# Kernel tuning notes

Measured on AMD Instinct MI355X. Metric: run time of the kernel, lower is better.

The kernel has to match this reference:

```python
import jax, jax.numpy as jnp
import numpy as np

EP = 1e-4
MAX_ITER = 100
L = [512, 512]          # context lengths
C = 256                 # padded feature dim == total_dim
HEADS = 2


def nonsat_activation(x, ep=EP, max_iter=MAX_ITER):
    # Fixed-point iteration y <- (2y^3/3 + x)/(y^2+1), y0 = x.
    # Matches torch version: iterate on detached values, final update uses live x.
    xd = jax.lax.stop_gradient(x)
    f = lambda y: (2.0 * y ** 3 / 3.0 + xd) / (y ** 2 + 1.0)

    def cond(s):
        y, y_new, i = s
        return jnp.logical_and(jnp.mean(jnp.abs(y_new - y)) > ep, i <= max_iter)

    def body(s):
        y, y_new, i = s
        return (y_new, f(y_new), i + 1)

    y_prev, _, _ = jax.lax.while_loop(cond, body, (xd, f(xd), 0))
    y_prev = jax.lax.stop_gradient(y_prev)
    # final (returned) update, differentiable w.r.t. x only
    return (2.0 * y_prev ** 3 / 3.0 + x) / (y_prev ** 2 + 1.0)


def setup_inputs() -> dict:
    key = jax.random.key(0)
    k1, k2, k3 = jax.random.split(key, 3)
    x1 = jax.random.normal(k1, (32, 512, 256), dtype=jnp.float32)
    x2 = jax.random.normal(k2, (32, 512, 192), dtype=jnp.float32)
    # xavier_normal_ for U: std = sqrt(2/(fan_in+fan_out)) = sqrt(2/512) = 1/16
    U = jax.random.normal(k3, (HEADS, C, C), dtype=jnp.float32) * (1.0 / 16.0)
    return {"x1": x1, "x2": x2, "U": U}


def reference(x1, x2, U):
    # pad contexts to common feature dim C (zeros on the right)
    contexts = [x1, jnp.pad(x2, ((0, 0), (0, 0), (0, C - x2.shape[-1])))]
    q = sum(L)
    scaling = C ** (-0.5)
    M = jnp.concatenate(contexts, axis=1)  # (B, q, C)

    # mask uses sizes = L[1:] with blocks starting at offset 0 (faithful quirk)
    mask_mul = jnp.ones((q, q), dtype=jnp.float32).at[:L[1], :L[1]].set(0.0)

    h_reps = []
    mask_add = None
    for h in range(HEADS):
        # K[b,i,j] = sum_{c,d} M[b,i,c] U[h,c,d] M[b,j,d]
        K = jnp.einsum('bic,cd,bjd->bij', M, U[h], M) * scaling
        K = nonsat_activation(K)
        if mask_add is None:  # cached after head 0, reused for later heads
            mask_add = jnp.zeros((q, q), dtype=jnp.float32).at[:L[1], :L[1]].set(jnp.min(K))
        K_hat = K * mask_mul + mask_add
        cols = jnp.max(K_hat, axis=1)   # (B, q) max over rows per column
        rows = jnp.max(K_hat, axis=2)   # (B, q) max over cols per row
        alpha = rows + cols             # (B, q)
        reps = []
        offset = 0
        for i, Ci in enumerate(contexts):
            a = alpha[:, offset:offset + L[i]]          # (B, l_i)
            offset += L[i]
            wt = jax.nn.softmax(a, axis=1)              # (B, l_i)
            r = jnp.einsum('bl,blc->bc', wt, Ci)        # (B, C)
            reps.append(r)
        h_reps.append(jnp.stack(reps, axis=1))          # (B, N, C)
    return jnp.stack(h_reps, axis=0)                    # (heads, B, N, C)
```

## Files before the change

### kernel.cpp

```cpp
#include <hip/hip_runtime.h>
#include <math.h>

typedef _Float16 h16;
typedef h16  h16x8 __attribute__((ext_vector_type(8)));
typedef h16  h16x4 __attribute__((ext_vector_type(4)));
typedef float f32x4 __attribute__((ext_vector_type(4)));

#define MH_OFF   ((size_t)0)
#define ML_OFF   (MH_OFF + 16777216)
#define UHT_OFF  (ML_OFF + 16777216)
#define ULT_OFF  (UHT_OFF + 262144)
#define RMA_OFF  (ULT_OFF + 262144)
#define RMH_OFF  (RMA_OFF + 262144)
#define PCM_OFF  (RMH_OFF + 262144)
#define M0_OFF   (PCM_OFF + 4194304)

__device__ __forceinline__ float nonsat(float x) {
    float y = x;
#pragma unroll
    for (int i = 0; i < 24; ++i) {
        float y2 = y * y;
        y = fmaf(0.66666667f * y, y2, x) / (y2 + 1.0f);
    }
    return y;
}

__device__ __forceinline__ int fkey(float f) {
    const int i = __float_as_int(f);
    return (i >= 0) ? i : (i ^ 0x7fffffff);
}
__device__ __forceinline__ float funkey(int k) {
    return __int_as_float((k >= 0) ? k : (k ^ 0x7fffffff));
}

__global__ void k_prep(const float* __restrict__ x1, const float* __restrict__ x2,
                       const float* __restrict__ U, h16* __restrict__ MH,
                       h16* __restrict__ ML, h16* __restrict__ UHt,
                       h16* __restrict__ ULt, int* __restrict__ m0key,
                       float* __restrict__ out) {
    const int gid = blockIdx.x * 256 + threadIdx.x;
    if (blockIdx.x < 8192) {
        const int g  = gid;
        const int d4 = (g & 63) * 4;
        const int j  = (g >> 6) & 1023;
        const int b  = g >> 16;
        float v[4];
        if (j < 512) {
            const float4 p = *(const float4*)(x1 + ((size_t)(b * 512 + j) * 256 + d4));
            v[0] = p.x; v[1] = p.y; v[2] = p.z; v[3] = p.w;
        } else if (d4 < 192) {
            const float4 p = *(const float4*)(x2 +
                (size_t)(b * 512 + (j - 512)) * 192 + d4);
            v[0] = p.x; v[1] = p.y; v[2] = p.z; v[3] = p.w;
        } else {
            v[0] = v[1] = v[2] = v[3] = 0.0f;
        }
        h16x4 hh, ll;
#pragma unroll
        for (int k = 0; k < 4; ++k) {
            const h16 hi = (h16)v[k];
            hh[k] = hi;
            ll[k] = (h16)(v[k] - (float)hi);
        }
        const size_t o = (size_t)g * 4;
        *(h16x4*)&MH[o] = hh;
        *(h16x4*)&ML[o] = ll;
    } else if (blockIdx.x < 8320) {
        const int g  = gid - 8192 * 256;
        const int c4 = (g & 63) * 4;
        const int d  = (g >> 6) & 255;
        const int h  = g >> 14;
        h16x4 hh, ll;
#pragma unroll
        for (int k = 0; k < 4; ++k) {
            const float v = U[((size_t)h * 256 + c4 + k) * 256 + d] * 4.0f;
            const h16 hi = (h16)v;
            hh[k] = hi;
            ll[k] = (h16)(v - (float)hi);
        }
        const size_t o = ((size_t)h * 256 + d) * 256 + c4;
        *(h16x4*)&UHt[o] = hh;
        *(h16x4*)&ULt[o] = ll;
    } else {
        const int z = gid - 8320 * 256;
        out[z] = 0.0f;
        if (z == 0) *m0key = 0x7fffffff;
    }
}

__global__ __launch_bounds__(256, 2)
void k_main(const h16* __restrict__ MH, const h16* __restrict__ ML,
            const h16* __restrict__ UHt, const h16* __restrict__ ULt,
            float* __restrict__ rmax_all, float* __restrict__ rmax_hi,
            float* __restrict__ pcm, int* __restrict__ m0key) {
    __shared__ __align__(16) h16 sP[2][64 * 256];
    __shared__ float red[512 + 4];

    const int n    = blockIdx.x;
    const int x    = n & 7;
    const int s    = n >> 3;
    const int b    = x + 8 * (s >> 5);
    const int h    = (s >> 4) & 1;
    const int rblk = s & 15;
    const int hb   = h * 32 + b;
    const int r0   = rblk * 64;
    const int t    = threadIdx.x;
    const int w    = t >> 6;
    const int l    = t & 63;
    const int q    = l >> 4;
    const int ln   = l & 15;
    const int phase = (w + s) & 3;

    {
        f32x4 acc[4][4];
        const f32x4 z4 = {0.f, 0.f, 0.f, 0.f};
#pragma unroll
        for (int i = 0; i < 4; ++i)
#pragma unroll
            for (int j = 0; j < 4; ++j) acc[i][j] = z4;

        for (int kcl = 0; kcl < 8; ++kcl) {
            const int kc = (kcl + phase * 2) & 7;
            const int c0 = kc * 32;
            h16x8 aH[4], aL[4], bH[4], bL[4];
#pragma unroll
            for (int ti = 0; ti < 4; ++ti) {
                const size_t off =
                    (size_t)(b * 1024 + r0 + ti * 16 + ln) * 256 + c0 + q * 8;
                aH[ti] = *(const h16x8*)&MH[off];
                aL[ti] = *(const h16x8*)&ML[off];
            }
#pragma unroll
            for (int tj = 0; tj < 4; ++tj) {
                const size_t off =
                    (size_t)(h * 256 + w * 64 + tj * 16 + ln) * 256 + c0 + q * 8;
                bH[tj] = *(const h16x8*)&UHt[off];
                bL[tj] = *(const h16x8*)&ULt[off];
            }
#pragma unroll
            for (int ti = 0; ti < 4; ++ti)
#pragma unroll
                for (int tj = 0; tj < 4; ++tj)
                    acc[ti][tj] = __builtin_amdgcn_mfma_f32_16x16x32_f16(
                        aH[ti], bH[tj], acc[ti][tj], 0, 0, 0);
#pragma unroll
            for (int ti = 0; ti < 4; ++ti)
#pragma unroll
                for (int tj = 0; tj < 4; ++tj)
                    acc[ti][tj] = __builtin_amdgcn_mfma_f32_16x16x32_f16(
                        aL[ti], bH[tj], acc[ti][tj], 0, 0, 0);
#pragma unroll
            for (int ti = 0; ti < 4; ++ti)
#pragma unroll
                for (int tj = 0; tj < 4; ++tj)
                    acc[ti][tj] = __builtin_amdgcn_mfma_f32_16x16x32_f16(
                        aH[ti], bL[tj], acc[ti][tj], 0, 0, 0);
        }
#pragma unroll
        for (int ti = 0; ti < 4; ++ti)
#pragma unroll
            for (int tj = 0; tj < 4; ++tj)
#pragma unroll
                for (int reg = 0; reg < 4; ++reg) {
                    const int r = ti * 16 + q * 4 + reg;
                    const int d = w * 64 + tj * 16 + ln;
                    const float v = acc[ti][tj][reg];
                    const h16 hi = (h16)v;
                    const h16 lo = (h16)(v - (float)hi);
                    const int off = r * 256 + (((d >> 3) ^ (r & 7)) << 3) + (d & 7);
                    sP[0][off] = hi;
                    sP[1][off] = lo;
                }
    }
    __syncthreads();

    float gmin = INFINITY;

    for (int jtl = 0; jtl < 2; ++jtl) {
        const int jt = (jtl + (phase & 1)) & 1;
        const int jbase = jt * 512 + w * 128;
        f32x4 acc[4][8];
        const f32x4 z4 = {0.f, 0.f, 0.f, 0.f};
#pragma unroll
        for (int i = 0; i < 4; ++i)
#pragma unroll
            for (int j = 0; j < 8; ++j) acc[i][j] = z4;

        for (int kcl = 0; kcl < 8; ++kcl) {
            const int kc = (kcl + phase * 2) & 7;
            const int d0 = kc * 32;
            h16x8 aH[4], aL[4], bb[8];
#pragma unroll
            for (int ti = 0; ti < 4; ++ti) {
                const int r = ti * 16 + ln;
                const int g = (kc * 4 + q) ^ (r & 7);
                aH[ti] = *(const h16x8*)&sP[0][r * 256 + g * 8];
                aL[ti] = *(const h16x8*)&sP[1][r * 256 + g * 8];
            }
#pragma unroll
            for (int tj = 0; tj < 8; ++tj)
                bb[tj] = *(const h16x8*)&MH[
                    (size_t)(b * 1024 + jbase + tj * 16 + ln) * 256 + d0 + q * 8];
#pragma unroll
            for (int tj = 0; tj < 8; ++tj)
#pragma unroll
                for (int ti = 0; ti < 4; ++ti)
                    acc[ti][tj] = __builtin_amdgcn_mfma_f32_16x16x32_f16(
                        aH[ti], bb[tj], acc[ti][tj], 0, 0, 0);
#pragma unroll
            for (int tj = 0; tj < 8; ++tj)
#pragma unroll
                for (int ti = 0; ti < 4; ++ti)
                    acc[ti][tj] = __builtin_amdgcn_mfma_f32_16x16x32_f16(
                        aL[ti], bb[tj], acc[ti][tj], 0, 0, 0);
#pragma unroll
            for (int tj = 0; tj < 8; ++tj)
                bb[tj] = *(const h16x8*)&ML[
                    (size_t)(b * 1024 + jbase + tj * 16 + ln) * 256 + d0 + q * 8];
#pragma unroll
            for (int tj = 0; tj < 8; ++tj)
#pragma unroll
                for (int ti = 0; ti < 4; ++ti)
                    acc[ti][tj] = __builtin_amdgcn_mfma_f32_16x16x32_f16(
                        aH[ti], bb[tj], acc[ti][tj], 0, 0, 0);
        }

#pragma unroll
        for (int ti = 0; ti < 4; ++ti)
#pragma unroll
            for (int reg = 0; reg < 4; ++reg) {
                float m = acc[ti][0][reg];
#pragma unroll
                for (int tj = 1; tj < 8; ++tj) m = fmaxf(m, acc[ti][tj][reg]);
                m = fmaxf(m, __shfl_xor(m, 1));
                m = fmaxf(m, __shfl_xor(m, 2));
                m = fmaxf(m, __shfl_xor(m, 4));
                m = fmaxf(m, __shfl_xor(m, 8));
                if (ln == 0)
                    red[(jt * 4 + w) * 64 + ti * 16 + q * 4 + reg] = m;
            }
#pragma unroll
        for (int tj = 0; tj < 8; ++tj) {
            float m = -INFINITY;
#pragma unroll
            for (int ti = 0; ti < 4; ++ti)
#pragma unroll
                for (int reg = 0; reg < 4; ++reg) m = fmaxf(m, acc[ti][tj][reg]);
            m = fmaxf(m, __shfl_xor(m, 16));
            m = fmaxf(m, __shfl_xor(m, 32));
            if (q == 0)
                pcm[(size_t)(hb * 16 + rblk) * 1024 + jbase + tj * 16 + ln] =
                    m * 0.015625f;
        }
#pragma unroll
        for (int ti = 0; ti < 4; ++ti)
#pragma unroll
            for (int tj = 0; tj < 8; ++tj)
#pragma unroll
                for (int reg = 0; reg < 4; ++reg)
                    gmin = fminf(gmin, acc[ti][tj][reg]);
    }

#pragma unroll
    for (int off = 1; off < 64; off <<= 1) gmin = fminf(gmin, __shfl_xor(gmin, off));
    if (l == 0) red[512 + w] = gmin;
    __syncthreads();

    if (t < 64) {
        float a = -INFINITY, hh = -INFINITY;
#pragma unroll
        for (int w2 = 0; w2 < 4; ++w2) {
            a  = fmaxf(a,  red[w2 * 64 + t]);
            const float v1 = red[(4 + w2) * 64 + t];
            a  = fmaxf(a, v1);
            hh = fmaxf(hh, v1);
        }
        rmax_all[(size_t)hb * 1024 + r0 + t] = a  * 0.015625f;
        rmax_hi [(size_t)hb * 1024 + r0 + t] = hh * 0.015625f;
    }
    if (t == 0 && hb < 32) {
        const float g4 = fminf(fminf(red[512], red[513]),
                               fminf(red[514], red[515])) * 0.015625f;
        atomicMin(m0key, fkey(g4));
    }
}

__global__ __launch_bounds__(256)
void k_fin(const float* __restrict__ rmax_all, const float* __restrict__ rmax_hi,
           const float* __restrict__ pcm, const int* __restrict__ m0key,
           const float* __restrict__ x1, const float* __restrict__ x2,
           float* __restrict__ out) {
    __shared__ float wv[512];
    __shared__ float sm[4], ss[4];
    const int blk   = blockIdx.x;
    const int chunk = blk & 1;
    const int seg   = (blk >> 1) & 1;
    const int hb    = blk >> 2;
    const int b     = hb & 31;
    const int t     = threadIdx.x;
    const float m0  = funkey(*m0key);

    float a2[2];
#pragma unroll
    for (int half = 0; half < 2; ++half) {
        const int i = seg * 512 + half * 256 + t;
        float rraw;
        if (seg == 0) rraw = fmaxf(m0, rmax_hi[(size_t)hb * 1024 + i]);
        else          rraw = rmax_all[(size_t)hb * 1024 + i];
        float call = -INFINITY, chi = -INFINITY;
#pragma unroll
        for (int rb = 0; rb < 16; ++rb) {
            const float v = pcm[(size_t)(hb * 16 + rb) * 1024 + i];
            call = fmaxf(call, v);
            if (rb >= 8) chi = fmaxf(chi, v);
        }
        const float craw = (seg == 0) ? fmaxf(m0, chi) : call;
        a2[half] = nonsat(rraw) + nonsat(craw);
    }
    const float a0 = a2[0], a1 = a2[1];

    float m = fmaxf(a0, a1);
#pragma unroll
    for (int off = 1; off < 64; off <<= 1) m = fmaxf(m, __shfl_xor(m, off));
    if ((t & 63) == 0) sm[t >> 6] = m;
    __syncthreads();
    const float amax = fmaxf(fmaxf(sm[0], sm[1]), fmaxf(sm[2], sm[3]));

    const float e0 = __expf(a0 - amax), e1 = __expf(a1 - amax);
    wv[t] = e0; wv[t + 256] = e1;
    float s = e0 + e1;
#pragma unroll
    for (int off = 1; off < 64; off <<= 1) s += __shfl_xor(s, off);
    if ((t & 63) == 0) ss[t >> 6] = s;
    __syncthreads();
    const float inv = 1.0f / (ss[0] + ss[1] + ss[2] + ss[3]);

    const int lo = chunk * 256;
    float acc = 0.0f;
    if (seg == 0) {
        const float* xp = x1 + ((size_t)b * 512 + lo) * 256 + t;
#pragma unroll 4
        for (int l = 0; l < 256; ++l)
            acc = fmaf(wv[lo + l], xp[(size_t)l * 256], acc);
        atomicAdd(&out[(hb * 2 + seg) * 256 + t], acc * inv);
    } else if (t < 192) {
        const float* xp = x2 + ((size_t)b * 512 + lo) * 192 + t;
#pragma unroll 4
        for (int l = 0; l < 256; ++l)
            acc = fmaf(wv[lo + l], xp[(size_t)l * 192], acc);
        atomicAdd(&out[(hb * 2 + seg) * 256 + t], acc * inv);
    }
}

extern "C" void kernel_launch(void* const* d_in, const int* in_sizes, int n_in,
                              void* d_out, int out_size, void* d_ws, size_t ws_size,
                              hipStream_t stream) {
    const float* x1 = (const float*)d_in[0];
    const float* x2 = (const float*)d_in[1];
    const float* U  = (const float*)d_in[2];
    float* out = (float*)d_out;
    char* wsb  = (char*)d_ws;

    h16*   MHp  = (h16*)(wsb + MH_OFF);
    h16*   MLp  = (h16*)(wsb + ML_OFF);
    h16*   UHt  = (h16*)(wsb + UHT_OFF);
    h16*   ULt  = (h16*)(wsb + ULT_OFF);
    float* rma  = (float*)(wsb + RMA_OFF);
    float* rmh  = (float*)(wsb + RMH_OFF);
    float* pcm  = (float*)(wsb + PCM_OFF);
    int*   m0k  = (int*)(wsb + M0_OFF);

    hipLaunchKernelGGL(k_prep, dim3(8448), dim3(256), 0, stream, x1, x2, U,
                       MHp, MLp, UHt, ULt, m0k, out);
    hipLaunchKernelGGL(k_main, dim3(1024), dim3(256), 0, stream, MHp, MLp,
                       UHt, ULt, rma, rmh, pcm, m0k);
    hipLaunchKernelGGL(k_fin,  dim3(256),  dim3(256), 0, stream, rma, rmh,
                       pcm, m0k, x1, x2, out);
}
```

Measured before the change: 287.1 us.

## Software-pipeline global loads in both GEMM phases and retile column loop

Both matrix-product phases of the main kernel now double-buffer register fragments: the next k-chunk's global loads are issued before the MFMAs on the current chunk, and in phase two the first chunk of the next column tile is prefetched as well. The second phase now walks four 64-column tiles per warp instead of two 128-column tiles. Row maxima are kept in registers across tiles and reduced once at the end, replacing the per-tile shuffle and shared-memory writes. The per-wave rotation of k-chunk order is removed. The extra prefetch buffers raise register pressure against the two-blocks-per-CU launch bound, and the loss of the staggered k order may increase cache contention.

```diff
diff --git a/kernel.cpp b/kernel.cpp
--- a/kernel.cpp
+++ b/kernel.cpp
@@ -88,6 +88,70 @@
     }
 }
 
+#define PA_LOAD(KC, AH_, AL_, BH_, BL_) {                                     \
+    const int c0_ = (KC) * 32;                                                \
+    _Pragma("unroll")                                                         \
+    for (int ti = 0; ti < 4; ++ti) {                                          \
+        const size_t off_ =                                                   \
+            (size_t)(b * 1024 + r0 + ti * 16 + ln) * 256 + c0_ + q * 8;       \
+        AH_[ti] = *(const h16x8*)&MH[off_];                                   \
+        AL_[ti] = *(const h16x8*)&ML[off_];                                   \
+    }                                                                         \
+    _Pragma("unroll")                                                         \
+    for (int tj = 0; tj < 4; ++tj) {                                          \
+        const size_t off_ =                                                   \
+            (size_t)(h * 256 + w * 64 + tj * 16 + ln) * 256 + c0_ + q * 8;    \
+        BH_[tj] = *(const h16x8*)&UHt[off_];                                  \
+        BL_[tj] = *(const h16x8*)&ULt[off_];                                  \
+    } }
+
+#define PA_MFMA(AH_, AL_, BH_, BL_) {                                         \
+    _Pragma("unroll") for (int ti = 0; ti < 4; ++ti)                          \
+    _Pragma("unroll") for (int tj = 0; tj < 4; ++tj)                          \
+        acc[ti][tj] = __builtin_amdgcn_mfma_f32_16x16x32_f16(                 \
+            AH_[ti], BH_[tj], acc[ti][tj], 0, 0, 0);                          \
+    _Pragma("unroll") for (int ti = 0; ti < 4; ++ti)                          \
+    _Pragma("unroll") for (int tj = 0; tj < 4; ++tj)                          \
+        acc[ti][tj] = __builtin_amdgcn_mfma_f32_16x16x32_f16(                 \
+            AL_[ti], BH_[tj], acc[ti][tj], 0, 0, 0);                          \
+    _Pragma("unroll") for (int ti = 0; ti < 4; ++ti)                          \
+    _Pragma("unroll") for (int tj = 0; tj < 4; ++tj)                          \
+        acc[ti][tj] = __builtin_amdgcn_mfma_f32_16x16x32_f16(                 \
+            AH_[ti], BL_[tj], acc[ti][tj], 0, 0, 0); }
+
+#define PB_LOAD(JB, KC, BH_, BL_) {                                           \
+    const int d0_ = (KC) * 32;                                                \
+    _Pragma("unroll")                                                         \
+    for (int tj = 0; tj < 4; ++tj) {                                          \
+        const size_t off_ =                                                   \
+            (size_t)(b * 1024 + (JB) + tj * 16 + ln) * 256 + d0_ + q * 8;     \
+        BH_[tj] = *(const h16x8*)&MH[off_];                                   \
+        BL_[tj] = *(const h16x8*)&ML[off_];                                   \
+    } }
+
+#define PB_LDSA(KC) {                                                         \
+    _Pragma("unroll")                                                         \
+    for (int ti = 0; ti < 4; ++ti) {                                          \
+        const int r_ = ti * 16 + ln;                                          \
+        const int g_ = ((KC) * 4 + q) ^ (r_ & 7);                             \
+        aH[ti] = *(const h16x8*)&sP[0][r_ * 256 + g_ * 8];                    \
+        aL[ti] = *(const h16x8*)&sP[1][r_ * 256 + g_ * 8];                    \
+    } }
+
+#define PB_MFMA(BH_, BL_) {                                                   \
+    _Pragma("unroll") for (int tj = 0; tj < 4; ++tj)                          \
+    _Pragma("unroll") for (int ti = 0; ti < 4; ++ti)                          \
+        acc[ti][tj] = __builtin_amdgcn_mfma_f32_16x16x32_f16(                 \
+            aH[ti], BH_[tj], acc[ti][tj], 0, 0, 0);                           \
+    _Pragma("unroll") for (int tj = 0; tj < 4; ++tj)                          \
+    _Pragma("unroll") for (int ti = 0; ti < 4; ++ti)                          \
+        acc[ti][tj] = __builtin_amdgcn_mfma_f32_16x16x32_f16(                 \
+            aL[ti], BH_[tj], acc[ti][tj], 0, 0, 0);                           \
+    _Pragma("unroll") for (int tj = 0; tj < 4; ++tj)                          \
+    _Pragma("unroll") for (int ti = 0; ti < 4; ++ti)                          \
+        acc[ti][tj] = __builtin_amdgcn_mfma_f32_16x16x32_f16(                 \
+            aH[ti], BL_[tj], acc[ti][tj], 0, 0, 0); }
+
 __global__ __launch_bounds__(256, 2)
 void k_main(const h16* __restrict__ MH, const h16* __restrict__ ML,
             const h16* __restrict__ UHt, const h16* __restrict__ ULt,
@@ -109,7 +173,6 @@
     const int l    = t & 63;
     const int q    = l >> 4;
     const int ln   = l & 15;
-    const int phase = (w + s) & 3;
 
     {
         f32x4 acc[4][4];
@@ -119,42 +182,15 @@
 #pragma unroll
             for (int j = 0; j < 4; ++j) acc[i][j] = z4;
 
-        for (int kcl = 0; kcl < 8; ++kcl) {
-            const int kc = (kcl + phase * 2) & 7;
-            const int c0 = kc * 32;
-            h16x8 aH[4], aL[4], bH[4], bL[4];
-#pragma unroll
-            for (int ti = 0; ti < 4; ++ti) {
-                const size_t off =
-                    (size_t)(b * 1024 + r0 + ti * 16 + ln) * 256 + c0 + q * 8;
-                aH[ti] = *(const h16x8*)&MH[off];
-                aL[ti] = *(const h16x8*)&ML[off];
-            }
-#pragma unroll
-            for (int tj = 0; tj < 4; ++tj) {
-                const size_t off =
-                    (size_t)(h * 256 + w * 64 + tj * 16 + ln) * 256 + c0 + q * 8;
-                bH[tj] = *(const h16x8*)&UHt[off];
-                bL[tj] = *(const h16x8*)&ULt[off];
-            }
-#pragma unroll
-            for (int ti = 0; ti < 4; ++ti)
-#pragma unroll
-                for (int tj = 0; tj < 4; ++tj)
-                    acc[ti][tj] = __builtin_amdgcn_mfma_f32_16x16x32_f16(
-                        aH[ti], bH[tj], acc[ti][tj], 0, 0, 0);
-#pragma unroll
-            for (int ti = 0; ti < 4; ++ti)
-#pragma unroll
-                for (int tj = 0; tj < 4; ++tj)
-                    acc[ti][tj] = __builtin_amdgcn_mfma_f32_16x16x32_f16(
-                        aL[ti], bH[tj], acc[ti][tj], 0, 0, 0);
-#pragma unroll
-            for (int ti = 0; ti < 4; ++ti)
-#pragma unroll
-                for (int tj = 0; tj < 4; ++tj)
-                    acc[ti][tj] = __builtin_amdgcn_mfma_f32_16x16x32_f16(
-                        aH[ti], bL[tj], acc[ti][tj], 0, 0, 0);
+        h16x8 A0[4], A0l[4], B0[4], B0l[4];
+        h16x8 A1[4], A1l[4], B1[4], B1l[4];
+        PA_LOAD(0, A0, A0l, B0, B0l);
+#pragma unroll
+        for (int kc2 = 0; kc2 < 8; kc2 += 2) {
+            PA_LOAD(kc2 + 1, A1, A1l, B1, B1l);
+            PA_MFMA(A0, A0l, B0, B0l);
+            if (kc2 + 2 < 8) { PA_LOAD(kc2 + 2, A0, A0l, B0, B0l); }
+            PA_MFMA(A1, A1l, B1, B1l);
         }
 #pragma unroll
         for (int ti = 0; ti < 4; ++ti)
@@ -174,73 +210,53 @@
     }
     __syncthreads();
 
+    float rA[16], rH[16];
+#pragma unroll
+    for (int i = 0; i < 16; ++i) { rA[i] = -INFINITY; rH[i] = -INFINITY; }
     float gmin = INFINITY;
 
-    for (int jtl = 0; jtl < 2; ++jtl) {
-        const int jt = (jtl + (phase & 1)) & 1;
-        const int jbase = jt * 512 + w * 128;
-        f32x4 acc[4][8];
+    h16x8 b0H[4], b0L[4], b1H[4], b1L[4], aH[4], aL[4];
+    PB_LOAD(w * 64, 0, b0H, b0L);
+
+#pragma unroll 1
+    for (int jt = 0; jt < 4; ++jt) {
+        const int jbase = jt * 256 + w * 64;
+        f32x4 acc[4][4];
         const f32x4 z4 = {0.f, 0.f, 0.f, 0.f};
 #pragma unroll
         for (int i = 0; i < 4; ++i)
 #pragma unroll
-            for (int j = 0; j < 8; ++j) acc[i][j] = z4;
-
-        for (int kcl = 0; kcl < 8; ++kcl) {
-            const int kc = (kcl + phase * 2) & 7;
-            const int d0 = kc * 32;
-            h16x8 aH[4], aL[4], bb[8];
-#pragma unroll
-            for (int ti = 0; ti < 4; ++ti) {
-                const int r = ti * 16 + ln;
-                const int g = (kc * 4 + q) ^ (r & 7);
-                aH[ti] = *(const h16x8*)&sP[0][r * 256 + g * 8];
-                aL[ti] = *(const h16x8*)&sP[1][r * 256 + g * 8];
+            for (int j = 0; j < 4; ++j) acc[i][j] = z4;
+
+#pragma unroll
+        for (int kc2 = 0; kc2 < 8; kc2 += 2) {
+            PB_LOAD(jbase, kc2 + 1, b1H, b1L);
+            PB_LDSA(kc2);
+            PB_MFMA(b0H, b0L);
+            if (kc2 + 2 < 8) {
+                PB_LOAD(jbase, kc2 + 2, b0H, b0L);
+            } else if (jt < 3) {
+                PB_LOAD(jbase + 256, 0, b0H, b0L);
             }
-#pragma unroll
-            for (int tj = 0; tj < 8; ++tj)
-                bb[tj] = *(const h16x8*)&MH[
-                    (size_t)(b * 1024 + jbase + tj * 16 + ln) * 256 + d0 + q * 8];
-#pragma unroll
-            for (int tj = 0; tj < 8; ++tj)
-#pragma unroll
-                for (int ti = 0; ti < 4; ++ti)
-                    acc[ti][tj] = __builtin_amdgcn_mfma_f32_16x16x32_f16(
-                        aH[ti], bb[tj], acc[ti][tj], 0, 0, 0);
-#pragma unroll
-            for (int tj = 0; tj < 8; ++tj)
-#pragma unroll
-                for (int ti = 0; ti < 4; ++ti)
-                    acc[ti][tj] = __builtin_amdgcn_mfma_f32_16x16x32_f16(
-                        aL[ti], bb[tj], acc[ti][tj], 0, 0, 0);
-#pragma unroll
-            for (int tj = 0; tj < 8; ++tj)
-                bb[tj] = *(const h16x8*)&ML[
-                    (size_t)(b * 1024 + jbase + tj * 16 + ln) * 256 + d0 + q * 8];
-#pragma unroll
-            for (int tj = 0; tj < 8; ++tj)
-#pragma unroll
-                for (int ti = 0; ti < 4; ++ti)
-                    acc[ti][tj] = __builtin_amdgcn_mfma_f32_16x16x32_f16(
-                        aH[ti], bb[tj], acc[ti][tj], 0, 0, 0);
-        }
-
+            PB_LDSA(kc2 + 1);
+            PB_MFMA(b1H, b1L);
+        }
+
+        const bool hij = (jt >= 2);
 #pragma unroll
         for (int ti = 0; ti < 4; ++ti)
 #pragma unroll
             for (int reg = 0; reg < 4; ++reg) {
                 float m = acc[ti][0][reg];
-#pragma unroll
-                for (int tj = 1; tj < 8; ++tj) m = fmaxf(m, acc[ti][tj][reg]);
-                m = fmaxf(m, __shfl_xor(m, 1));
-                m = fmaxf(m, __shfl_xor(m, 2));
-                m = fmaxf(m, __shfl_xor(m, 4));
-                m = fmaxf(m, __shfl_xor(m, 8));
-                if (ln == 0)
-                    red[(jt * 4 + w) * 64 + ti * 16 + q * 4 + reg] = m;
+                m = fmaxf(m, acc[ti][1][reg]);
+                m = fmaxf(m, acc[ti][2][reg]);
+                m = fmaxf(m, acc[ti][3][reg]);
+                const int idx = ti * 4 + reg;
+                rA[idx] = fmaxf(rA[idx], m);
+                if (hij) rH[idx] = fmaxf(rH[idx], m);
             }
 #pragma unroll
-        for (int tj = 0; tj < 8; ++tj) {
+        for (int tj = 0; tj < 4; ++tj) {
             float m = -INFINITY;
 #pragma unroll
             for (int ti = 0; ti < 4; ++ti)
@@ -255,12 +271,29 @@
 #pragma unroll
         for (int ti = 0; ti < 4; ++ti)
 #pragma unroll
-            for (int tj = 0; tj < 8; ++tj)
+            for (int tj = 0; tj < 4; ++tj)
 #pragma unroll
                 for (int reg = 0; reg < 4; ++reg)
                     gmin = fminf(gmin, acc[ti][tj][reg]);
     }
 
+#pragma unroll
+    for (int ti = 0; ti < 4; ++ti)
+#pragma unroll
+        for (int reg = 0; reg < 4; ++reg) {
+            const int idx = ti * 4 + reg;
+            float a = rA[idx], hh = rH[idx];
+#pragma unroll
+            for (int o2 = 1; o2 < 16; o2 <<= 1) {
+                a  = fmaxf(a,  __shfl_xor(a,  o2));
+                hh = fmaxf(hh, __shfl_xor(hh, o2));
+            }
+            if (ln == 0) {
+                const int row = ti * 16 + q * 4 + reg;
+                red[w * 64 + row]       = a;
+                red[256 + w * 64 + row] = hh;
+            }
+        }
 #pragma unroll
     for (int off = 1; off < 64; off <<= 1) gmin = fminf(gmin, __shfl_xor(gmin, off));
     if (l == 0) red[512 + w] = gmin;
@@ -271,9 +304,7 @@
 #pragma unroll
         for (int w2 = 0; w2 < 4; ++w2) {
             a  = fmaxf(a,  red[w2 * 64 + t]);
-            const float v1 = red[(4 + w2) * 64 + t];
-            a  = fmaxf(a, v1);
-            hh = fmaxf(hh, v1);
+            hh = fmaxf(hh, red[256 + w2 * 64 + t]);
         }
         rmax_all[(size_t)hb * 1024 + r0 + t] = a  * 0.015625f;
         rmax_hi [(size_t)hb * 1024 + r0 + t] = hh * 0.015625f;
```

New measurement: 412.8 us. 1.44x slower.
